# Performance work log

Measured on AMD Instinct MI355X. Metric: run time of the kernel, lower is better.

The kernel has to match this reference:

```python
import jax, jax.numpy as jnp
import numpy as np
import math

B, T, C = 4, 2048, 768
N_HEAD = 12
HEAD_DIM = C // N_HEAD


def setup_inputs() -> dict:
    key = jax.random.key(0)
    k1, k2, k3, k4, k5 = jax.random.split(key, 5)
    std = 0.02
    x = jax.random.normal(k1, (B, T, C), dtype=jnp.float32)
    W_attn = jax.random.normal(k2, (C, 3 * C), dtype=jnp.float32) * std
    b_attn = jnp.zeros((3 * C,), dtype=jnp.float32)
    W_proj = jax.random.normal(k3, (C, C), dtype=jnp.float32) * std
    b_proj = jnp.zeros((C,), dtype=jnp.float32)
    return {"x": x, "W_attn": W_attn, "b_attn": b_attn,
            "W_proj": W_proj, "b_proj": b_proj}


def reference(x, W_attn, b_attn, W_proj, b_proj):
    b, t, c = x.shape
    h, hd = N_HEAD, c // N_HEAD
    # qkv projection: [B,T,3C] -> q,k,v each [B,H,T,hd]
    qkv = x @ W_attn + b_attn
    qkv = qkv.reshape(b, t, 3, h, hd).transpose(2, 0, 3, 1, 4)  # [3,B,H,T,hd]
    q, k, v = qkv[0], qkv[1], qkv[2]
    scale = 1.0 / math.sqrt(hd)
    # full T x T attention scores (non-flash, as in original)
    attn = jnp.einsum('bhqd,bhkd->bhqk', q, k) * scale  # [B,H,T,T]
    causal = jnp.tril(jnp.ones((t, t), dtype=bool))
    attn = jnp.where(causal[None, None, :, :], attn, -jnp.inf)
    attn = jax.nn.softmax(attn, axis=-1)
    y = jnp.einsum('bhqk,bhkd->bhqd', attn, v)  # [B,H,T,hd]
    y = y.transpose(0, 2, 1, 3).reshape(b, t, c)  # merge heads
    return y @ W_proj + b_proj
```

## Files before the change

### kernel.cpp

```cpp
#include <hip/hip_runtime.h>
#include <hip/hip_bf16.h>
#include <cstdint>

#define B_  4
#define T_  2048
#define C_  768
#define H_  12
#define HD_ 64

#define AS1 __attribute__((address_space(1)))
#define AS3 __attribute__((address_space(3)))

typedef float    f32x4  __attribute__((ext_vector_type(4)));
typedef __bf16   bf16x8 __attribute__((ext_vector_type(8)));
typedef uint32_t u32x4  __attribute__((ext_vector_type(4)));

#define QSCL 0.18033688011112042f
#define MFIX 8.0f

__device__ __forceinline__ uint16_t f2b(float f) {
  __bf16 h = (__bf16)f;
  return __builtin_bit_cast(uint16_t, h);
}
__device__ __forceinline__ uint32_t pk2(float a, float b) {
  return (uint32_t)f2b(a) | ((uint32_t)f2b(b) << 16);
}

__global__ void k_cvt(const float* __restrict__ in, uint16_t* __restrict__ out, int n4) {
  int i = blockIdx.x * blockDim.x + threadIdx.x;
  if (i >= n4) return;
  float4 v = ((const float4*)in)[i];
  uint2 o;
  o.x = pk2(v.x, v.y);
  o.y = pk2(v.z, v.w);
  ((uint2*)out)[i] = o;
}

__global__ void k_tr2(const float* __restrict__ Wa, uint16_t* __restrict__ WtA,
                      const float* __restrict__ Wp, uint16_t* __restrict__ WtP) {
  __shared__ float tile[32][33];
  const int bx = blockIdx.x;
  const float* in;
  uint16_t* out;
  int Cc, n0;
  if (bx < 72) { in = Wa; out = WtA; Cc = 2304; n0 = bx * 32; }
  else         { in = Wp; out = WtP; Cc = 768;  n0 = (bx - 72) * 32; }
  const int k0 = blockIdx.y * 32;
  const int tx = threadIdx.x, ty = threadIdx.y;
#pragma unroll
  for (int i = 0; i < 32; i += 8)
    tile[ty + i][tx] = in[(size_t)(k0 + ty + i) * Cc + n0 + tx];
  __syncthreads();
#pragma unroll
  for (int i = 0; i < 32; i += 8)
    out[(size_t)(n0 + ty + i) * 768 + k0 + tx] = f2b(tile[tx][ty + i]);
}

template <int EPI>
__global__ __launch_bounds__(256, 3) void k_gemm(
    const uint16_t* __restrict__ A, const uint16_t* __restrict__ Bt,
    const float* __restrict__ bias, float* __restrict__ outF,
    uint16_t* __restrict__ outQKV, int M, int N, int K, int nY) {
  __shared__ __align__(16) uint16_t As[2][128 * 32];
  __shared__ __align__(16) uint16_t Bs[2][128 * 32];
  const int nwg = gridDim.x;
  const int bid = blockIdx.x;
  const int wgid = (bid & 7) * (nwg >> 3) + (bid >> 3);
  const int wy = wgid % nY, wx = wgid / nY;

  const int tid  = threadIdx.x;
  const int lane = tid & 63;
  const int wave = tid >> 6;
  const int wrow = (wave >> 1) * 64, wcol = (wave & 1) * 64;
  const int rowBase = wx * 128, colBase = wy * 128;
  const int l16 = lane & 15, kg = lane >> 4;

  f32x4 acc[4][4];
#pragma unroll
  for (int i = 0; i < 4; ++i)
#pragma unroll
    for (int j = 0; j < 4; ++j) acc[i][j] = (f32x4){0.f, 0.f, 0.f, 0.f};

  const int srow  = lane >> 2;
  const int sslot = lane & 3;
  const int ssw   = (sslot ^ (srow & 3)) << 3;

  auto STAGE = [&](int buf, int k0) {
#pragma unroll
    for (int i = 0; i < 2; ++i) {
      const int r = i * 64 + wave * 16 + srow;
      const uint16_t* srcA = A  + (size_t)(rowBase + r) * K + k0 + ssw;
      const uint16_t* srcB = Bt + (size_t)(colBase + r) * K + k0 + ssw;
      uint16_t* dstA = &As[buf][(i * 64 + wave * 16) * 32];
      uint16_t* dstB = &Bs[buf][(i * 64 + wave * 16) * 32];
      __builtin_amdgcn_global_load_lds((const AS1 uint32_t*)srcA, (AS3 uint32_t*)dstA, 16, 0, 0);
      __builtin_amdgcn_global_load_lds((const AS1 uint32_t*)srcB, (AS3 uint32_t*)dstB, 16, 0, 0);
    }
  };

  const int sA = (kg ^ (l16 & 3)) << 3;

  STAGE(0, 0);
  int cur = 0;
  for (int k0 = 0; k0 < K; k0 += 32) {
    __syncthreads();
    if (k0 + 32 < K) STAGE(cur ^ 1, k0 + 32);
    bf16x8 af[4], bfv[4];
#pragma unroll
    for (int mi = 0; mi < 4; ++mi)
      af[mi] = *(const bf16x8*)&As[cur][(wrow + mi * 16 + l16) * 32 + sA];
#pragma unroll
    for (int nj = 0; nj < 4; ++nj)
      bfv[nj] = *(const bf16x8*)&Bs[cur][(wcol + nj * 16 + l16) * 32 + sA];
#pragma unroll
    for (int mi = 0; mi < 4; ++mi)
#pragma unroll
      for (int nj = 0; nj < 4; ++nj)
        acc[mi][nj] = __builtin_amdgcn_mfma_f32_16x16x32_bf16(af[mi], bfv[nj], acc[mi][nj], 0, 0, 0);
    cur ^= 1;
  }

  const int rg = lane >> 4;
#pragma unroll
  for (int mi = 0; mi < 4; ++mi)
#pragma unroll
    for (int nj = 0; nj < 4; ++nj) {
      int c = colBase + wcol + nj * 16 + l16;
      float bv = bias[c];
#pragma unroll
      for (int jj = 0; jj < 4; ++jj) {
        int r = rowBase + wrow + mi * 16 + rg * 4 + jj;
        float v = acc[mi][nj][jj] + bv;
        if (EPI == 0) {
          outF[(size_t)r * N + c] = v;
        } else {
          int sel = c / 768;
          int rem = c - sel * 768;
          int head = rem >> 6, d = rem & 63;
          int bb = r >> 11, tt = r & 2047;
          size_t off;
          if (sel == 2)
            off = (((size_t)2 * (B_ * H_) + bb * H_ + head) * HD_ + d) * T_ + tt;
          else
            off = (((size_t)sel * (B_ * H_) + bb * H_ + head) * T_ + tt) * HD_ + d;
          if (sel == 0) v *= QSCL;
          outQKV[off] = f2b(v);
        }
      }
    }
}

__global__ __launch_bounds__(256, 4) void k_attn2(
    const uint16_t* __restrict__ Qb, const uint16_t* __restrict__ Kb,
    const uint16_t* __restrict__ Vb, uint16_t* __restrict__ Y) {
  __shared__ __align__(16) uint16_t Ks[2][64 * 64];
  __shared__ __align__(16) uint16_t Vs[2][64 * 64];
  __shared__ __align__(16) uint16_t Ps[4][16 * 64];
  const int tid  = threadIdx.x;
  const int lane = tid & 63;
  const int wq   = tid >> 6;
  const int l16  = lane & 15, kg = lane >> 4;

  const int idx = blockIdx.x;
  const int tq  = idx >> 3;
  const int px  = tq & 15;
  const int g   = (idx & 7) + 8 * (tq >> 4);
  const int h = g % H_, b = g / H_;
  const size_t headBase = ((size_t)(b * H_ + h)) * (size_t)(T_ * HD_);

  const int srow0 = wq * 16 + (lane >> 3);
  const int sslot = lane & 7;
  const int swz = (l16 & 7) << 2;

  uint32_t* pwords = (uint32_t*)&Ps[wq][0];

  auto STAGE = [&](int buf, int t) {
    const int kvoff = t * 64;
#pragma unroll
    for (int j = 0; j < 2; ++j) {
      const int r  = srow0 + j * 8;
      const int sw = ((sslot ^ (r & 7)) << 3);
      const uint16_t* srcK = Kb + headBase + (size_t)(kvoff + r) * HD_ + sw;
      const uint16_t* srcV = Vb + headBase + (size_t)r * T_ + kvoff + sw;
      uint16_t* dstK = &Ks[buf][(wq * 16 + j * 8) * 64];
      uint16_t* dstV = &Vs[buf][(wq * 16 + j * 8) * 64];
      __builtin_amdgcn_global_load_lds((const AS1 uint32_t*)srcK, (AS3 uint32_t*)dstK, 16, 0, 0);
      __builtin_amdgcn_global_load_lds((const AS1 uint32_t*)srcV, (AS3 uint32_t*)dstV, 16, 0, 0);
    }
  };

  int cur = 0;
  for (int part = 0; part < 2; ++part) {
    const int qb = part ? (31 - px) : px;
    const int qrow0 = qb * 64 + wq * 16;

    bf16x8 qf[2];
    {
      const uint16_t* qp = Qb + headBase + (size_t)(qrow0 + l16) * HD_;
      qf[0] = *(const bf16x8*)(qp + kg * 8);
      qf[1] = *(const bf16x8*)(qp + 32 + kg * 8);
    }

    f32x4 o[4];
#pragma unroll
    for (int i = 0; i < 4; ++i) o[i] = (f32x4){0.f, 0.f, 0.f, 0.f};
    f32x4 lacc = (f32x4){0.f, 0.f, 0.f, 0.f};

    const int nt = qb + 1;
    __syncthreads();
    STAGE(cur, 0);

    for (int t = 0; t < nt; ++t) {
      __syncthreads();
      if (t + 1 < nt) STAGE(cur ^ 1, t + 1);

      const uint16_t* KT = &Ks[cur][0];
      const uint16_t* VT = &Vs[cur][0];

      f32x4 sm[4];
      __builtin_amdgcn_s_setprio(1);
#pragma unroll
      for (int nj = 0; nj < 4; ++nj) {
        f32x4 acc = (f32x4){0.f, 0.f, 0.f, 0.f};
#pragma unroll
        for (int kc = 0; kc < 2; ++kc) {
          const int row = nj * 16 + l16;
          const int s = (((kc * 4 + kg) ^ (row & 7)) << 3);
          bf16x8 kf = *(const bf16x8*)&KT[row * 64 + s];
          acc = __builtin_amdgcn_mfma_f32_16x16x32_bf16(kf, qf[kc], acc, 0, 0, 0);
        }
        sm[nj] = acc;
      }
      __builtin_amdgcn_s_setprio(0);

      if (t == qb) {
        const int kvb = t * 64 + kg * 4;
        const int qg  = qrow0 + l16;
#pragma unroll
        for (int nj = 0; nj < 4; ++nj)
#pragma unroll
          for (int jj = 0; jj < 4; ++jj)
            if (kvb + nj * 16 + jj > qg) sm[nj][jj] = -__builtin_inff();
      }

#pragma unroll
      for (int nj = 0; nj < 4; ++nj) {
#pragma unroll
        for (int jj = 0; jj < 4; ++jj)
          sm[nj][jj] = __builtin_exp2f(sm[nj][jj] - MFIX);
        lacc += sm[nj];
      }

#pragma unroll
      for (int nj = 0; nj < 4; ++nj) {
        uint2 w;
        w.x = pk2(sm[nj][0], sm[nj][1]);
        w.y = pk2(sm[nj][2], sm[nj][3]);
        const int cs = (nj * 8 + kg * 2) ^ swz;
        *(uint2*)&pwords[l16 * 32 + cs] = w;
      }

      __builtin_amdgcn_s_setprio(1);
#pragma unroll
      for (int kc = 0; kc < 2; ++kc) {
        const int cr = (kc * 16 + kg * 4) ^ swz;
        bf16x8 pa = *(const bf16x8*)&pwords[l16 * 32 + cr];
#pragma unroll
        for (int njd = 0; njd < 4; ++njd) {
          const int row = njd * 16 + l16;
          const int s = (((kc * 4 + kg) ^ (row & 7)) << 3);
          bf16x8 vf = *(const bf16x8*)&VT[row * 64 + s];
          o[njd] = __builtin_amdgcn_mfma_f32_16x16x32_bf16(vf, pa, o[njd], 0, 0, 0);
        }
      }
      __builtin_amdgcn_s_setprio(0);

      cur ^= 1;
    }

    float l_ = (lacc[0] + lacc[1]) + (lacc[2] + lacc[3]);
    l_ += __shfl_xor(l_, 16);
    l_ += __shfl_xor(l_, 32);
    float inv = __builtin_amdgcn_rcpf(l_);
    const int q = qrow0 + l16;
    uint16_t* yp = Y + ((size_t)(b * T_ + q)) * C_ + h * HD_ + kg * 4;
#pragma unroll
    for (int njd = 0; njd < 4; ++njd) {
      uint2 w;
      w.x = pk2(o[njd][0] * inv, o[njd][1] * inv);
      w.y = pk2(o[njd][2] * inv, o[njd][3] * inv);
      *(uint2*)(yp + njd * 16) = w;
    }
  }
}

extern "C" void kernel_launch(void* const* d_in, const int* in_sizes, int n_in,
                              void* d_out, int out_size, void* d_ws, size_t ws_size,
                              hipStream_t stream) {
  const float* x      = (const float*)d_in[0];
  const float* W_attn = (const float*)d_in[1];
  const float* b_attn = (const float*)d_in[2];
  const float* W_proj = (const float*)d_in[3];
  const float* b_proj = (const float*)d_in[4];
  float* out = (float*)d_out;

  char* ws = (char*)d_ws;
  uint16_t* xb  = (uint16_t*)(ws);
  uint16_t* WtA = (uint16_t*)(ws + 12582912);
  uint16_t* WtP = (uint16_t*)(ws + 16121856);
  uint16_t* QKV = (uint16_t*)(ws + 17301504);
  uint16_t* Yb  = (uint16_t*)(ws + 55050240);

  uint16_t* Qp = QKV;
  uint16_t* Kp = QKV + 6291456;
  uint16_t* Vp = QKV + 12582912;

  k_cvt<<<6144, 256, 0, stream>>>(x, xb, 1572864);
  k_tr2<<<dim3(96, 24), dim3(32, 8), 0, stream>>>(W_attn, WtA, W_proj, WtP);
  k_gemm<1><<<1152, 256, 0, stream>>>(xb, WtA, b_attn, nullptr, QKV, 8192, 2304, 768, 18);
  k_attn2<<<768, 256, 0, stream>>>(Qp, Kp, Vp, Yb);
  k_gemm<0><<<384, 256, 0, stream>>>(Yb, WtP, b_proj, out, nullptr, 8192, 768, 768, 6);
}
```

Before: 158.2 us.

## Triple-buffer GEMM LDS staging with explicit vmcnt waits and vectorize V-store epilogue

```diff
diff --git a/kernel.cpp b/kernel.cpp
--- a/kernel.cpp
+++ b/kernel.cpp
@@ -61,8 +61,8 @@
     const uint16_t* __restrict__ A, const uint16_t* __restrict__ Bt,
     const float* __restrict__ bias, float* __restrict__ outF,
     uint16_t* __restrict__ outQKV, int M, int N, int K, int nY) {
-  __shared__ __align__(16) uint16_t As[2][128 * 32];
-  __shared__ __align__(16) uint16_t Bs[2][128 * 32];
+  __shared__ __align__(16) uint16_t As[3][128 * 32];
+  __shared__ __align__(16) uint16_t Bs[3][128 * 32];
   const int nwg = gridDim.x;
   const int bid = blockIdx.x;
   const int wgid = (bid & 7) * (nwg >> 3) + (bid >> 3);
@@ -101,23 +101,35 @@
   const int sA = (kg ^ (l16 & 3)) << 3;
 
   STAGE(0, 0);
-  int cur = 0;
-  for (int k0 = 0; k0 < K; k0 += 32) {
-    __syncthreads();
-    if (k0 + 32 < K) STAGE(cur ^ 1, k0 + 32);
+  if (32 < K) STAGE(1, 32);
+  int t = 0;
+  for (int k0 = 0; k0 < K; k0 += 32, ++t) {
+    if (k0 + 64 < K) {
+      STAGE((t + 2) % 3, k0 + 64);
+      asm volatile("s_waitcnt vmcnt(8)" ::: "memory");
+    } else if (k0 + 32 < K) {
+      asm volatile("s_waitcnt vmcnt(4)" ::: "memory");
+    } else {
+      asm volatile("s_waitcnt vmcnt(0)" ::: "memory");
+    }
+    __builtin_amdgcn_sched_barrier(0);
+    __builtin_amdgcn_s_barrier();
+
+    const int cb = t % 3;
     bf16x8 af[4], bfv[4];
 #pragma unroll
     for (int mi = 0; mi < 4; ++mi)
-      af[mi] = *(const bf16x8*)&As[cur][(wrow + mi * 16 + l16) * 32 + sA];
+      af[mi] = *(const bf16x8*)&As[cb][(wrow + mi * 16 + l16) * 32 + sA];
 #pragma unroll
     for (int nj = 0; nj < 4; ++nj)
-      bfv[nj] = *(const bf16x8*)&Bs[cur][(wcol + nj * 16 + l16) * 32 + sA];
+      bfv[nj] = *(const bf16x8*)&Bs[cb][(wcol + nj * 16 + l16) * 32 + sA];
 #pragma unroll
     for (int mi = 0; mi < 4; ++mi)
 #pragma unroll
       for (int nj = 0; nj < 4; ++nj)
         acc[mi][nj] = __builtin_amdgcn_mfma_f32_16x16x32_bf16(af[mi], bfv[nj], acc[mi][nj], 0, 0, 0);
-    cur ^= 1;
+
+    __builtin_amdgcn_s_barrier();
   }
 
   const int rg = lane >> 4;
@@ -127,24 +139,31 @@
     for (int nj = 0; nj < 4; ++nj) {
       int c = colBase + wcol + nj * 16 + l16;
       float bv = bias[c];
-#pragma unroll
-      for (int jj = 0; jj < 4; ++jj) {
-        int r = rowBase + wrow + mi * 16 + rg * 4 + jj;
-        float v = acc[mi][nj][jj] + bv;
-        if (EPI == 0) {
-          outF[(size_t)r * N + c] = v;
+      if (EPI == 0) {
+#pragma unroll
+        for (int jj = 0; jj < 4; ++jj) {
+          int r = rowBase + wrow + mi * 16 + rg * 4 + jj;
+          outF[(size_t)r * N + c] = acc[mi][nj][jj] + bv;
+        }
+      } else {
+        int sel = c / 768;
+        int rem = c - sel * 768;
+        int head = rem >> 6, d = rem & 63;
+        int r0 = rowBase + wrow + mi * 16 + rg * 4;
+        int bb = r0 >> 11, tt0 = r0 & 2047;
+        if (sel == 2) {
+          size_t off = (((size_t)2 * (B_ * H_) + bb * H_ + head) * HD_ + d) * T_ + tt0;
+          uint2 w;
+          w.x = pk2(acc[mi][nj][0] + bv, acc[mi][nj][1] + bv);
+          w.y = pk2(acc[mi][nj][2] + bv, acc[mi][nj][3] + bv);
+          *(uint2*)&outQKV[off] = w;
         } else {
-          int sel = c / 768;
-          int rem = c - sel * 768;
-          int head = rem >> 6, d = rem & 63;
-          int bb = r >> 11, tt = r & 2047;
-          size_t off;
-          if (sel == 2)
-            off = (((size_t)2 * (B_ * H_) + bb * H_ + head) * HD_ + d) * T_ + tt;
-          else
-            off = (((size_t)sel * (B_ * H_) + bb * H_ + head) * T_ + tt) * HD_ + d;
-          if (sel == 0) v *= QSCL;
-          outQKV[off] = f2b(v);
+          float scl = (sel == 0) ? QSCL : 1.0f;
+#pragma unroll
+          for (int jj = 0; jj < 4; ++jj) {
+            size_t off = (((size_t)sel * (B_ * H_) + bb * H_ + head) * T_ + tt0 + jj) * HD_ + d;
+            outQKV[off] = f2b((acc[mi][nj][jj] + bv) * scl);
+          }
         }
       }
     }
```

After: 139.9 us. 1.13x faster.
